# Optimization experiments

Measured on AMD Instinct MI355X. Metric: run time of the kernel, lower is better.

The kernel has to match this reference:

```python
import jax, jax.numpy as jnp
import numpy as np

N_NODES = 50000
N_EDGES = 800000
D = 64  # node_dim == edge_dim
NEG_SLOPE = 0.2
EPS = 1e-5


def _lin_params(key, d_in, d_out):
    k1, k2 = jax.random.split(key)
    bound = 1.0 / np.sqrt(d_in)
    W = jax.random.uniform(k1, (d_out, d_in), minval=-bound, maxval=bound, dtype=jnp.float32)
    b = jax.random.uniform(k2, (d_out,), minval=-bound, maxval=bound, dtype=jnp.float32)
    return W, b


def setup_inputs() -> dict:
    key = jax.random.key(0)
    ks = jax.random.split(key, 12)
    V = jax.random.normal(ks[0], (N_NODES, D), dtype=jnp.float32)
    E = jax.random.normal(ks[1], (N_EDGES, D), dtype=jnp.float32)
    src = jax.random.randint(ks[2], (N_EDGES,), 0, N_NODES, dtype=jnp.int32)
    dst = jax.random.randint(ks[3], (N_EDGES,), 0, N_NODES, dtype=jnp.int32)
    pA_w, pA_b = _lin_params(ks[4], D, D)   # NodePooling.A
    pB_w, pB_b = _lin_params(ks[5], D, D)   # NodePooling.B
    mW1, mb1 = _lin_params(ks[6], D, D)     # edge MLP layer 1
    mW2, mb2 = _lin_params(ks[7], D, D)     # edge MLP layer 2
    BW, Bb = _lin_params(ks[8], D, D)       # GenMessage.B (scale)
    CW, Cb = _lin_params(ks[9], D, D)       # GenMessage.C (shift)
    return {"V": V, "E": E, "src": src, "dst": dst,
            "pA_w": pA_w, "pA_b": pA_b, "pB_w": pB_w, "pB_b": pB_b,
            "mW1": mW1, "mb1": mb1, "mW2": mW2, "mb2": mb2,
            "BW": BW, "Bb": Bb, "CW": CW, "Cb": Cb}


def _lrelu(x):
    return jnp.where(x >= 0, x, NEG_SLOPE * x)


def reference(V, E, src, dst, pA_w, pA_b, pB_w, pB_b, mW1, mb1, mW2, mb2, BW, Bb, CW, Cb):
    n = V.shape[0]
    # V = act(V); NodePooling: B(lrelu(A(V)))
    Va = _lrelu(V)
    Vp = _lrelu(Va @ pA_w.T + pA_b) @ pB_w.T + pB_b  # [N, D]
    # edge MLP on edge features (2 Linear+ReLU layers)
    x = jax.nn.relu(E @ mW1.T + mb1)
    x = jax.nn.relu(x @ mW2.T + mb2)                  # [E, D]
    scale = jax.nn.sigmoid(x @ BW.T + Bb)
    shift = x @ CW.T + Cb
    # gathered src features, gated affine message
    M1 = scale * Vp[src] + shift                      # [E, D]
    M2 = M1 * M1
    # segment-mean onto dst (DGL fn.mean); zero for isolated nodes
    deg = jax.ops.segment_sum(jnp.ones((dst.shape[0],), jnp.float32), dst, num_segments=n)
    denom = jnp.maximum(deg, 1.0)[:, None]
    V1 = jax.ops.segment_sum(M1, dst, num_segments=n) / denom
    V2 = jax.ops.segment_sum(M2, dst, num_segments=n) / denom
    return jnp.sqrt(jax.nn.relu(V2 - V1) + EPS)
```

## Files before the change

kernel.cpp:

```cpp
#include <hip/hip_runtime.h>

#define NN 50000
#define NE 800000
#define DDIM 64
#define PADX 68
#define PADS 68
#define NB_SCAN ((NN + 255) / 256)
#define NEG_SLOPE 0.2f
#define EPS_V 1e-5f

typedef short bf16x8 __attribute__((ext_vector_type(8)));
typedef float f32x4 __attribute__((ext_vector_type(4)));

__device__ __forceinline__ float lrelu_f(float x) { return x >= 0.0f ? x : NEG_SLOPE * x; }

__device__ __forceinline__ unsigned short bf16_rn(float x) {
    union { float f; unsigned int u; } c; c.f = x;
    unsigned int r = c.u + 0x7FFF + ((c.u >> 16) & 1);
    return (unsigned short)(r >> 16);
}
__device__ __forceinline__ float bf16_tof(unsigned short h) {
    union { float f; unsigned int u; } c; c.u = ((unsigned int)h) << 16;
    return c.f;
}

__device__ __forceinline__ unsigned cvtpk_bf16(float a, float b) {
    unsigned r;
    asm("v_cvt_pk_bf16_f32 %0, %1, %2" : "=v"(r) : "v"(a), "v"(b));
    return r;
}

__device__ __forceinline__ void split8(const float* __restrict__ v, bf16x8& h, bf16x8& l)
{
    union { bf16x8 v8; unsigned u[4]; } H, L;
    #pragma unroll
    for (int k = 0; k < 4; ++k) {
        float a = v[2*k], b = v[2*k+1];
        unsigned p = cvtpk_bf16(a, b);
        union { float f; unsigned u; } h0, h1;
        h0.u = p << 16;
        h1.u = p & 0xFFFF0000u;
        unsigned q = cvtpk_bf16(a - h0.f, b - h1.f);
        H.u[k] = p;
        L.u[k] = q;
    }
    h = H.v8; l = L.v8;
}

__device__ __forceinline__ void mma_tile(float acc[16], const float* __restrict__ XT,
                                         const float* __restrict__ Wc, int e0, int f0)
{
    #pragma unroll 4
    for (int kk = 0; kk < DDIM; kk += 4) {
        float4 A0 = *(const float4*)&XT[(kk+0)*PADX + e0];
        float4 A1 = *(const float4*)&XT[(kk+1)*PADX + e0];
        float4 A2 = *(const float4*)&XT[(kk+2)*PADX + e0];
        float4 A3 = *(const float4*)&XT[(kk+3)*PADX + e0];
        float4 B0 = *(const float4*)&Wc[(f0+0)*PADX + kk];
        float4 B1 = *(const float4*)&Wc[(f0+1)*PADX + kk];
        float4 B2 = *(const float4*)&Wc[(f0+2)*PADX + kk];
        float4 B3 = *(const float4*)&Wc[(f0+3)*PADX + kk];
        const float a[4][4] = {{A0.x,A0.y,A0.z,A0.w},{A1.x,A1.y,A1.z,A1.w},
                               {A2.x,A2.y,A2.z,A2.w},{A3.x,A3.y,A3.z,A3.w}};
        const float b[4][4] = {{B0.x,B0.y,B0.z,B0.w},{B1.x,B1.y,B1.z,B1.w},
                               {B2.x,B2.y,B2.z,B2.w},{B3.x,B3.y,B3.z,B3.w}};
        #pragma unroll
        for (int j = 0; j < 4; ++j)
            #pragma unroll
            for (int i = 0; i < 4; ++i)
                #pragma unroll
                for (int q = 0; q < 4; ++q)
                    acc[i*4+j] = fmaf(a[q][i], b[j][q], acc[i*4+j]);
    }
}

__device__ __forceinline__ void load_w_f32(float* __restrict__ Wc, const float* __restrict__ Wg, int tid)
{
    #pragma unroll
    for (int c = 0; c < 4; ++c) {
        int idx = (c << 10) + (tid << 2);
        int f = idx >> 6, k = idx & 63;
        *(float4*)&Wc[f*PADX + k] = *(const float4*)&Wg[idx];
    }
}

__global__ __launch_bounds__(256, 3)
void node_pool_kernel(const float* __restrict__ V,
                      const float* __restrict__ Aw, const float* __restrict__ Ab,
                      const float* __restrict__ Bw, const float* __restrict__ Bbv,
                      float* __restrict__ Vp,
                      const int* __restrict__ dst, int* __restrict__ degi)
{
    __shared__ float Wc[DDIM*PADX];
    __shared__ float XT[DDIM*PADX];
    const int tid = threadIdx.x;
    const int nb = blockIdx.x * 64;
    const int e0 = (tid & 15) << 2;
    const int f0 = (tid >> 4) << 2;

    #pragma unroll
    for (int c = 0; c < 4; ++c) {
        int idx = (c << 10) + (tid << 2);
        int e = idx >> 6, d = idx & 63;
        int row = nb + e; if (row > NN-1) row = NN-1;
        float4 v = *(const float4*)&V[(size_t)row*DDIM + d];
        XT[(d+0)*PADX + e] = lrelu_f(v.x);
        XT[(d+1)*PADX + e] = lrelu_f(v.y);
        XT[(d+2)*PADX + e] = lrelu_f(v.z);
        XT[(d+3)*PADX + e] = lrelu_f(v.w);
    }
    load_w_f32(Wc, Aw, tid);
    __syncthreads();

    float acc[16];
    #pragma unroll
    for (int i = 0; i < 16; ++i) acc[i] = 0.f;
    mma_tile(acc, XT, Wc, e0, f0);
    __syncthreads();

    {
        float4 bv = *(const float4*)&Ab[f0];
        const float ba[4] = {bv.x, bv.y, bv.z, bv.w};
        #pragma unroll
        for (int j = 0; j < 4; ++j) {
            float4 v;
            v.x = lrelu_f(acc[0*4+j] + ba[j]);
            v.y = lrelu_f(acc[1*4+j] + ba[j]);
            v.z = lrelu_f(acc[2*4+j] + ba[j]);
            v.w = lrelu_f(acc[3*4+j] + ba[j]);
            *(float4*)&XT[(f0+j)*PADX + e0] = v;
        }
    }
    load_w_f32(Wc, Bw, tid);
    __syncthreads();

    float acc2[16];
    #pragma unroll
    for (int i = 0; i < 16; ++i) acc2[i] = 0.f;
    mma_tile(acc2, XT, Wc, e0, f0);

    float4 bv = *(const float4*)&Bbv[f0];
    #pragma unroll
    for (int i = 0; i < 4; ++i) {
        int row = nb + e0 + i;
        if (row < NN) {
            float4 o;
            o.x = acc2[i*4+0] + bv.x;
            o.y = acc2[i*4+1] + bv.y;
            o.z = acc2[i*4+2] + bv.z;
            o.w = acc2[i*4+3] + bv.w;
            *(float4*)&Vp[(size_t)row*DDIM + f0] = o;
        }
    }

    const int stride = gridDim.x * 256;
    for (int e = blockIdx.x * 256 + tid; e < NE; e += stride)
        atomicAdd(&degi[dst[e]], 1);
}

__global__ __launch_bounds__(256)
void prep_w_kernel(const float* __restrict__ W1, const float* __restrict__ W2,
                   const float* __restrict__ WB, const float* __restrict__ WC,
                   short* __restrict__ WF)
{
    int gid = blockIdx.x * 256 + threadIdx.x;
    int L = gid >> 12, r = gid & 4095;
    int t = r >> 10, ks = (r >> 9) & 1, lane = (r >> 3) & 63, j = r & 7;
    const float* Ws = (L == 0) ? W1 : (L == 1) ? W2 : (L == 2) ? WB : WC;
    int n = lane & 15, kg = lane >> 4;
    int f = t*16 + n, k = ks*32 + kg*8 + j;
    float v = Ws[f*64 + k];
    unsigned short h = bf16_rn(v);
    unsigned short l = bf16_rn(v - bf16_tof(h));
    int base = L*8192 + ((t*2 + ks)*2)*512 + lane*8 + j;
    WF[base]       = (short)h;
    WF[base + 512] = (short)l;
}

__global__ __launch_bounds__(256)
void scan1_kernel(const int* __restrict__ degi, int* __restrict__ linc, int* __restrict__ bsum)
{
    __shared__ int ws[4];
    const int tid = threadIdx.x;
    const int lane = tid & 63, wv = tid >> 6;
    int i = blockIdx.x * 256 + tid;
    int v = (i < NN) ? degi[i] : 0;
    int sc = v;
    #pragma unroll
    for (int off = 1; off < 64; off <<= 1) {
        int t = __shfl_up(sc, off, 64);
        if (lane >= off) sc += t;
    }
    if (lane == 63) ws[wv] = sc;
    __syncthreads();
    int wb = 0;
    #pragma unroll
    for (int w = 0; w < 4; ++w) if (w < wv) wb += ws[w];
    int incl = sc + wb;
    if (i < NN) linc[i] = incl;
    if (tid == 255) bsum[blockIdx.x] = incl;
}

__global__ __launch_bounds__(256)
void scan23_kernel(const int* __restrict__ degi, const int* __restrict__ linc,
                   const int* __restrict__ bsum, int* __restrict__ curs)
{
    __shared__ int ws[4];
    __shared__ int base_s;
    const int tid = threadIdx.x;
    const int lane = tid & 63, wv = tid >> 6;
    int v = (tid < NB_SCAN) ? bsum[tid] : 0;
    int sc = v;
    #pragma unroll
    for (int off = 1; off < 64; off <<= 1) {
        int t = __shfl_up(sc, off, 64);
        if (lane >= off) sc += t;
    }
    if (lane == 63) ws[wv] = sc;
    __syncthreads();
    int wb = 0;
    #pragma unroll
    for (int w = 0; w < 4; ++w) if (w < wv) wb += ws[w];
    if (tid == blockIdx.x) base_s = sc + wb - v;
    __syncthreads();
    int i = blockIdx.x * 256 + tid;
    if (i < NN) curs[i] = base_s + linc[i] - degi[i];
}

__global__ __launch_bounds__(256)
void scatter_kernel(const int* __restrict__ dst, int* __restrict__ cursor, int* __restrict__ eidx)
{
    int e = blockIdx.x * 256 + threadIdx.x;
    if (e < NE) {
        int p = atomicAdd(&cursor[dst[e]], 1);
        eidx[p] = e;
    }
}

__device__ __forceinline__ void gemm64_dual_lds(const short* bw, int lane,
                                                const bf16x8 ah0[2], const bf16x8 al0[2],
                                                const bf16x8 ah1[2], const bf16x8 al1[2],
                                                f32x4 acc0[4], f32x4 acc1[4])
{
    #pragma unroll
    for (int ks = 0; ks < 2; ++ks) {
        bf16x8 bh[4], bl[4];
        #pragma unroll
        for (int t = 0; t < 4; ++t) {
            bh[t] = *(const bf16x8*)&bw[(((t*2 + ks)*2 + 0)*64 + lane)*8];
            bl[t] = *(const bf16x8*)&bw[(((t*2 + ks)*2 + 1)*64 + lane)*8];
        }
        #pragma unroll
        for (int t = 0; t < 4; ++t) {
            acc0[t] = __builtin_amdgcn_mfma_f32_16x16x32_bf16(al0[ks], bh[t], acc0[t], 0, 0, 0);
            acc1[t] = __builtin_amdgcn_mfma_f32_16x16x32_bf16(al1[ks], bh[t], acc1[t], 0, 0, 0);
            acc0[t] = __builtin_amdgcn_mfma_f32_16x16x32_bf16(ah0[ks], bl[t], acc0[t], 0, 0, 0);
            acc1[t] = __builtin_amdgcn_mfma_f32_16x16x32_bf16(ah1[ks], bl[t], acc1[t], 0, 0, 0);
            acc0[t] = __builtin_amdgcn_mfma_f32_16x16x32_bf16(ah0[ks], bh[t], acc0[t], 0, 0, 0);
            acc1[t] = __builtin_amdgcn_mfma_f32_16x16x32_bf16(ah1[ks], bh[t], acc1[t], 0, 0, 0);
        }
    }
}

__device__ __forceinline__ void transpose_frags(float* __restrict__ sw, const f32x4 y[4],
                                                int lane, bf16x8 ah[2], bf16x8 al[2])
{
    const int n = lane & 15, mg = lane >> 4;
    #pragma unroll
    for (int t = 0; t < 4; ++t)
        #pragma unroll
        for (int r = 0; r < 4; ++r)
            sw[(mg*4 + r)*PADS + t*16 + n] = y[t][r];
    __builtin_amdgcn_wave_barrier();
    const int m = lane & 15, kg = lane >> 4;
    float x[16];
    *(float4*)&x[0]  = *(const float4*)&sw[m*PADS + kg*8];
    *(float4*)&x[4]  = *(const float4*)&sw[m*PADS + kg*8 + 4];
    *(float4*)&x[8]  = *(const float4*)&sw[m*PADS + 32 + kg*8];
    *(float4*)&x[12] = *(const float4*)&sw[m*PADS + 32 + kg*8 + 4];
    split8(&x[0], ah[0], al[0]);
    split8(&x[8], ah[1], al[1]);
    __builtin_amdgcn_wave_barrier();
}

__global__ __launch_bounds__(256, 3)
void edge_fused_kernel(const float* __restrict__ Eg,
                       const int* __restrict__ src, const int* __restrict__ dst,
                       const int* __restrict__ eidx,
                       const short* __restrict__ WF,
                       const float* __restrict__ b1, const float* __restrict__ b2,
                       const float* __restrict__ bB, const float* __restrict__ bC,
                       const float* __restrict__ Vp,
                       float* __restrict__ S1, float* __restrict__ S2)
{
    __shared__ short bw[8192];
    __shared__ float scratch[4 * 16 * PADS];
    __shared__ int aux[4 * 64];

    const int tid = threadIdx.x;
    const int lane = tid & 63, wv = tid >> 6;
    float* sw = scratch + wv * 16 * PADS;
    int* auxw = aux + wv * 64;

    const int ew = blockIdx.x * 128 + wv * 32;
    const int m = lane & 15, kg = lane >> 4;
    const int n = lane & 15, mg = lane >> 4;

    auto load_layer = [&](const short* Wg) {
        __syncthreads();
        const uint4* s = (const uint4*)Wg;
        uint4* d = (uint4*)bw;
        #pragma unroll
        for (int c = 0; c < 4; ++c)
            d[c*256 + tid] = s[c*256 + tid];
        __syncthreads();
    };

    if (lane < 32) {
        int eg = eidx[ew + lane];
        auxw[lane]      = src[eg];
        auxw[32 + lane] = dst[eg];
    }
    bf16x8 ah0[2], al0[2], ah1[2], al1[2];
    {
        int eg0 = eidx[ew + m];
        int eg1 = eidx[ew + 16 + m];
        const float* er0 = Eg + (size_t)eg0*DDIM + kg*8;
        const float* er1 = Eg + (size_t)eg1*DDIM + kg*8;
        float x[16];
        *(float4*)&x[0]  = *(const float4*)&er0[0];
        *(float4*)&x[4]  = *(const float4*)&er0[4];
        *(float4*)&x[8]  = *(const float4*)&er0[32];
        *(float4*)&x[12] = *(const float4*)&er0[36];
        split8(&x[0], ah0[0], al0[0]);
        split8(&x[8], ah0[1], al0[1]);
        *(float4*)&x[0]  = *(const float4*)&er1[0];
        *(float4*)&x[4]  = *(const float4*)&er1[4];
        *(float4*)&x[8]  = *(const float4*)&er1[32];
        *(float4*)&x[12] = *(const float4*)&er1[36];
        split8(&x[0], ah1[0], al1[0]);
        split8(&x[8], ah1[1], al1[1]);
    }

    load_layer(WF);
    f32x4 acc0[4], acc1[4];
    #pragma unroll
    for (int t = 0; t < 4; ++t) { acc0[t] = (f32x4){0.f,0.f,0.f,0.f}; acc1[t] = (f32x4){0.f,0.f,0.f,0.f}; }
    gemm64_dual_lds(bw, lane, ah0, al0, ah1, al1, acc0, acc1);
    #pragma unroll
    for (int t = 0; t < 4; ++t) {
        float b = b1[t*16 + n];
        #pragma unroll
        for (int r = 0; r < 4; ++r) {
            acc0[t][r] = fmaxf(acc0[t][r] + b, 0.0f);
            acc1[t][r] = fmaxf(acc1[t][r] + b, 0.0f);
        }
    }
    transpose_frags(sw, acc0, lane, ah0, al0);
    transpose_frags(sw, acc1, lane, ah1, al1);

    load_layer(WF + 8192);
    #pragma unroll
    for (int t = 0; t < 4; ++t) { acc0[t] = (f32x4){0.f,0.f,0.f,0.f}; acc1[t] = (f32x4){0.f,0.f,0.f,0.f}; }
    gemm64_dual_lds(bw, lane, ah0, al0, ah1, al1, acc0, acc1);
    #pragma unroll
    for (int t = 0; t < 4; ++t) {
        float b = b2[t*16 + n];
        #pragma unroll
        for (int r = 0; r < 4; ++r) {
            acc0[t][r] = fmaxf(acc0[t][r] + b, 0.0f);
            acc1[t][r] = fmaxf(acc1[t][r] + b, 0.0f);
        }
    }
    transpose_frags(sw, acc0, lane, ah0, al0);
    transpose_frags(sw, acc1, lane, ah1, al1);

    f32x4 accS0[4], accS1[4];
    load_layer(WF + 2*8192);
    #pragma unroll
    for (int t = 0; t < 4; ++t) { accS0[t] = (f32x4){0.f,0.f,0.f,0.f}; accS1[t] = (f32x4){0.f,0.f,0.f,0.f}; }
    gemm64_dual_lds(bw, lane, ah0, al0, ah1, al1, accS0, accS1);

    f32x4 accH0[4], accH1[4];
    load_layer(WF + 3*8192);
    #pragma unroll
    for (int t = 0; t < 4; ++t) { accH0[t] = (f32x4){0.f,0.f,0.f,0.f}; accH1[t] = (f32x4){0.f,0.f,0.f,0.f}; }
    gemm64_dual_lds(bw, lane, ah0, al0, ah1, al1, accH0, accH1);

    const int f = lane;
    float s1 = 0.f, s2 = 0.f;
    int prev = auxw[32];
    #pragma unroll
    for (int tile = 0; tile < 2; ++tile) {
        const int to = tile * 16;
        f32x4* accS = tile ? accS1 : accS0;
        f32x4* accH = tile ? accH1 : accH0;

        {
            int sn[4];
            #pragma unroll
            for (int r = 0; r < 4; ++r) sn[r] = auxw[to + mg*4 + r];
            #pragma unroll
            for (int t = 0; t < 4; ++t) {
                const int ff = t*16 + n;
                const float bBv = bB[ff];
                const float bCv = bC[ff];
                #pragma unroll
                for (int r = 0; r < 4; ++r) {
                    float vp = Vp[(size_t)sn[r]*DDIM + ff];
                    float sg = 1.0f / (1.0f + __expf(-(accS[t][r] + bBv)));
                    sw[(mg*4 + r)*PADS + ff] = fmaf(sg, vp, accH[t][r] + bCv);
                }
            }
        }
        __builtin_amdgcn_wave_barrier();

        #pragma unroll 4
        for (int e = 0; e < 16; ++e) {
            int dn = auxw[32 + to + e];
            float m1 = sw[e*PADS + f];
            float m2 = m1 * m1;
            if (dn != prev) {
                atomicAdd(&S1[(size_t)prev*DDIM + f], s1);
                atomicAdd(&S2[(size_t)prev*DDIM + f], s2);
                s1 = 0.f; s2 = 0.f; prev = dn;
            }
            s1 += m1; s2 += m2;
        }
        __builtin_amdgcn_wave_barrier();
    }
    atomicAdd(&S1[(size_t)prev*DDIM + f], s1);
    atomicAdd(&S2[(size_t)prev*DDIM + f], s2);
}

__global__ __launch_bounds__(256)
void finalize_kernel(const float* __restrict__ S1, const float* __restrict__ S2,
                     const int* __restrict__ degi, float* __restrict__ out)
{
    int gid = blockIdx.x * blockDim.x + threadIdx.x;
    if (gid >= NN*DDIM) return;
    int n = gid >> 6;
    float dn = (float)degi[n];
    dn = dn > 1.0f ? dn : 1.0f;
    float v = (S2[gid] - S1[gid]) / dn;
    out[gid] = sqrtf(fmaxf(v, 0.0f) + EPS_V);
}

extern "C" void kernel_launch(void* const* d_in, const int* in_sizes, int n_in,
                              void* d_out, int out_size, void* d_ws, size_t ws_size,
                              hipStream_t stream) {
    const float* V   = (const float*)d_in[0];
    const float* Eg  = (const float*)d_in[1];
    const int*   src = (const int*)d_in[2];
    const int*   dst = (const int*)d_in[3];
    const float* pAw = (const float*)d_in[4];
    const float* pAb = (const float*)d_in[5];
    const float* pBw = (const float*)d_in[6];
    const float* pBb = (const float*)d_in[7];
    const float* mW1 = (const float*)d_in[8];
    const float* mb1 = (const float*)d_in[9];
    const float* mW2 = (const float*)d_in[10];
    const float* mb2 = (const float*)d_in[11];
    const float* BW  = (const float*)d_in[12];
    const float* Bb  = (const float*)d_in[13];
    const float* CW  = (const float*)d_in[14];
    const float* Cb  = (const float*)d_in[15];
    float* out = (float*)d_out;

    float* ws    = (float*)d_ws;
    float* Vp    = ws;
    float* S1    = ws + (size_t)NN*DDIM;
    float* S2    = ws + (size_t)2*NN*DDIM;
    int*   degi  = (int*)(ws + (size_t)3*NN*DDIM);
    int*   curs  = degi + NN;
    int*   linc  = curs + NN;
    int*   bsum  = linc + NN;
    int*   eidx  = bsum + NB_SCAN;
    short* WF    = (short*)(eidx + NE);

    hipMemsetAsync(S1, 0, (size_t)(2*NN*DDIM + NN) * sizeof(float), stream);

    prep_w_kernel<<<64, 256, 0, stream>>>(mW1, mW2, BW, CW, WF);
    node_pool_kernel<<<(NN + 63)/64, 256, 0, stream>>>(V, pAw, pAb, pBw, pBb, Vp, dst, degi);
    scan1_kernel<<<NB_SCAN, 256, 0, stream>>>(degi, linc, bsum);
    scan23_kernel<<<NB_SCAN, 256, 0, stream>>>(degi, linc, bsum, curs);
    scatter_kernel<<<(NE + 255)/256, 256, 0, stream>>>(dst, curs, eidx);
    edge_fused_kernel<<<NE/128, 256, 0, stream>>>(Eg, src, dst, eidx, WF,
                                                  mb1, mb2, Bb, Cb, Vp, S1, S2);
    finalize_kernel<<<(NN*DDIM + 255)/256, 256, 0, stream>>>(S1, S2, degi, out);
}
```

Measured before the change: 505.8 us.

## Prefetch next layer weights into registers, merge weight prep into node pool

In the fused edge kernel, the next layer's bf16 weight tile is now loaded from global memory into registers while the current layer's MFMA GEMM runs, and only written to LDS between barriers. This hides the global load latency that was previously exposed inside each layer transition. The GEMMs are also wrapped in s_setprio to favour matrix work, and the separate weight-prep kernel is folded into extra blocks of the node-pool launch to save one launch. The cost is 16 extra VGPRs per thread held across each GEMM, which may reduce occupancy under the 3-blocks-per-SM launch bound.

```diff
diff --git a/kernel.cpp b/kernel.cpp
--- a/kernel.cpp
+++ b/kernel.cpp
@@ -6,6 +6,7 @@
 #define PADX 68
 #define PADS 68
 #define NB_SCAN ((NN + 255) / 256)
+#define NPB ((NN + 63) / 64)
 #define NEG_SLOPE 0.2f
 #define EPS_V 1e-5f
 
@@ -89,11 +90,35 @@
                       const float* __restrict__ Aw, const float* __restrict__ Ab,
                       const float* __restrict__ Bw, const float* __restrict__ Bbv,
                       float* __restrict__ Vp,
-                      const int* __restrict__ dst, int* __restrict__ degi)
+                      const int* __restrict__ dst, int* __restrict__ degi,
+                      const float* __restrict__ W1, const float* __restrict__ W2,
+                      const float* __restrict__ WB, const float* __restrict__ WC,
+                      short* __restrict__ WF)
 {
     __shared__ float Wc[DDIM*PADX];
     __shared__ float XT[DDIM*PADX];
     const int tid = threadIdx.x;
+
+    if (blockIdx.x >= NPB) {
+        int gid = (blockIdx.x - NPB) * 256 + tid;
+        int L = gid >> 12, r = gid & 4095;
+        int t = r >> 10, ks = (r >> 9) & 1, lane = (r >> 3) & 63, j = r & 7;
+        const float* Ws = (L == 0) ? W1 : (L == 1) ? W2 : (L == 2) ? WB : WC;
+        int n = lane & 15, kg = lane >> 4;
+        int f = t*16 + n, k = ks*32 + kg*8 + j;
+        float v = Ws[f*64 + k];
+        unsigned short h = bf16_rn(v);
+        unsigned short l = bf16_rn(v - bf16_tof(h));
+        int base = L*8192 + ((t*2 + ks)*2)*512 + lane*8 + j;
+        WF[base]       = (short)h;
+        WF[base + 512] = (short)l;
+
+        const int stride = gridDim.x * 256;
+        for (int e = blockIdx.x * 256 + tid; e < NE; e += stride)
+            atomicAdd(&degi[dst[e]], 1);
+        return;
+    }
+
     const int nb = blockIdx.x * 64;
     const int e0 = (tid & 15) << 2;
     const int f0 = (tid >> 4) << 2;
@@ -156,25 +181,6 @@
     const int stride = gridDim.x * 256;
     for (int e = blockIdx.x * 256 + tid; e < NE; e += stride)
         atomicAdd(&degi[dst[e]], 1);
-}
-
-__global__ __launch_bounds__(256)
-void prep_w_kernel(const float* __restrict__ W1, const float* __restrict__ W2,
-                   const float* __restrict__ WB, const float* __restrict__ WC,
-                   short* __restrict__ WF)
-{
-    int gid = blockIdx.x * 256 + threadIdx.x;
-    int L = gid >> 12, r = gid & 4095;
-    int t = r >> 10, ks = (r >> 9) & 1, lane = (r >> 3) & 63, j = r & 7;
-    const float* Ws = (L == 0) ? W1 : (L == 1) ? W2 : (L == 2) ? WB : WC;
-    int n = lane & 15, kg = lane >> 4;
-    int f = t*16 + n, k = ks*32 + kg*8 + j;
-    float v = Ws[f*64 + k];
-    unsigned short h = bf16_rn(v);
-    unsigned short l = bf16_rn(v - bf16_tof(h));
-    int base = L*8192 + ((t*2 + ks)*2)*512 + lane*8 + j;
-    WF[base]       = (short)h;
-    WF[base + 512] = (short)l;
 }
 
 __global__ __launch_bounds__(256)
@@ -293,7 +299,7 @@
                        const float* __restrict__ Vp,
                        float* __restrict__ S1, float* __restrict__ S2)
 {
-    __shared__ short bw[8192];
+    __shared__ __align__(16) short bw[8192];
     __shared__ float scratch[4 * 16 * PADS];
     __shared__ int aux[4 * 64];
 
@@ -306,15 +312,14 @@
     const int m = lane & 15, kg = lane >> 4;
     const int n = lane & 15, mg = lane >> 4;
 
-    auto load_layer = [&](const short* Wg) {
-        __syncthreads();
-        const uint4* s = (const uint4*)Wg;
-        uint4* d = (uint4*)bw;
-        #pragma unroll
-        for (int c = 0; c < 4; ++c)
-            d[c*256 + tid] = s[c*256 + tid];
-        __syncthreads();
-    };
+    uint4 w0, w1, w2, w3;
+    #define ISSUE_W(Wg) do { const uint4* s_ = (const uint4*)(Wg); \
+        w0 = s_[tid]; w1 = s_[256 + tid]; w2 = s_[512 + tid]; w3 = s_[768 + tid]; } while (0)
+    #define COMMIT_W() do { __syncthreads(); uint4* d_ = (uint4*)bw; \
+        d_[tid] = w0; d_[256 + tid] = w1; d_[512 + tid] = w2; d_[768 + tid] = w3; \
+        __syncthreads(); } while (0)
+
+    ISSUE_W(WF);
 
     if (lane < 32) {
         int eg = eidx[ew + lane];
@@ -342,11 +347,14 @@
         split8(&x[8], ah1[1], al1[1]);
     }
 
-    load_layer(WF);
+    COMMIT_W();
+    ISSUE_W(WF + 8192);
     f32x4 acc0[4], acc1[4];
     #pragma unroll
     for (int t = 0; t < 4; ++t) { acc0[t] = (f32x4){0.f,0.f,0.f,0.f}; acc1[t] = (f32x4){0.f,0.f,0.f,0.f}; }
+    __builtin_amdgcn_s_setprio(1);
     gemm64_dual_lds(bw, lane, ah0, al0, ah1, al1, acc0, acc1);
+    __builtin_amdgcn_s_setprio(0);
     #pragma unroll
     for (int t = 0; t < 4; ++t) {
         float b = b1[t*16 + n];
@@ -359,10 +367,13 @@
     transpose_frags(sw, acc0, lane, ah0, al0);
     transpose_frags(sw, acc1, lane, ah1, al1);
 
-    load_layer(WF + 8192);
+    COMMIT_W();
+    ISSUE_W(WF + 2*8192);
     #pragma unroll
     for (int t = 0; t < 4; ++t) { acc0[t] = (f32x4){0.f,0.f,0.f,0.f}; acc1[t] = (f32x4){0.f,0.f,0.f,0.f}; }
+    __builtin_amdgcn_s_setprio(1);
     gemm64_dual_lds(bw, lane, ah0, al0, ah1, al1, acc0, acc1);
+    __builtin_amdgcn_s_setprio(0);
     #pragma unroll
     for (int t = 0; t < 4; ++t) {
         float b = b2[t*16 + n];
@@ -375,17 +386,22 @@
     transpose_frags(sw, acc0, lane, ah0, al0);
     transpose_frags(sw, acc1, lane, ah1, al1);
 
+    COMMIT_W();
+    ISSUE_W(WF + 3*8192);
     f32x4 accS0[4], accS1[4];
-    load_layer(WF + 2*8192);
     #pragma unroll
     for (int t = 0; t < 4; ++t) { accS0[t] = (f32x4){0.f,0.f,0.f,0.f}; accS1[t] = (f32x4){0.f,0.f,0.f,0.f}; }
+    __builtin_amdgcn_s_setprio(1);
     gemm64_dual_lds(bw, lane, ah0, al0, ah1, al1, accS0, accS1);
-
+    __builtin_amdgcn_s_setprio(0);
+
+    COMMIT_W();
     f32x4 accH0[4], accH1[4];
-    load_layer(WF + 3*8192);
     #pragma unroll
     for (int t = 0; t < 4; ++t) { accH0[t] = (f32x4){0.f,0.f,0.f,0.f}; accH1[t] = (f32x4){0.f,0.f,0.f,0.f}; }
+    __builtin_amdgcn_s_setprio(1);
     gemm64_dual_lds(bw, lane, ah0, al0, ah1, al1, accH0, accH1);
+    __builtin_amdgcn_s_setprio(0);
 
     const int f = lane;
     float s1 = 0.f, s2 = 0.f;
@@ -431,6 +447,8 @@
     }
     atomicAdd(&S1[(size_t)prev*DDIM + f], s1);
     atomicAdd(&S2[(size_t)prev*DDIM + f], s2);
+    #undef ISSUE_W
+    #undef COMMIT_W
 }
 
 __global__ __launch_bounds__(256)
@@ -480,8 +498,8 @@
 
     hipMemsetAsync(S1, 0, (size_t)(2*NN*DDIM + NN) * sizeof(float), stream);
 
-    prep_w_kernel<<<64, 256, 0, stream>>>(mW1, mW2, BW, CW, WF);
-    node_pool_kernel<<<(NN + 63)/64, 256, 0, stream>>>(V, pAw, pAb, pBw, pBb, Vp, dst, degi);
+    node_pool_kernel<<<NPB + 64, 256, 0, stream>>>(V, pAw, pAb, pBw, pBb, Vp, dst, degi,
+                                                   mW1, mW2, BW, CW, WF);
     scan1_kernel<<<NB_SCAN, 256, 0, stream>>>(degi, linc, bsum);
     scan23_kernel<<<NB_SCAN, 256, 0, stream>>>(degi, linc, bsum, curs);
     scatter_kernel<<<(NE + 255)/256, 256, 0, stream>>>(dst, curs, eidx);
```

Measured after the change: 491.3 us (median of 4 runs). -2.9%, faster.
